# Optimization experiments

Hardware: AMD Instinct MI355X
Metric: run time of the kernel (lower is better)

## Reference

```python
import jax, jax.numpy as jnp
import numpy as np

B, S, HIDDEN = 4, 2048, 1024
NUM_EXPERTS = 8
TOP_K = 4
EPS = 1e-6


def setup_inputs() -> dict:
    key = jax.random.key(0)
    k0, k1, k2 = jax.random.split(key, 3)
    x = jax.random.normal(k0, (B, S, HIDDEN), dtype=jnp.float32)
    Wg = jax.random.normal(k1, (HIDDEN, NUM_EXPERTS), dtype=jnp.float32) * 0.02
    bg = jnp.zeros((NUM_EXPERTS,), dtype=jnp.float32)
    W = jax.random.normal(k2, (NUM_EXPERTS, HIDDEN, HIDDEN), dtype=jnp.float32) * 0.02
    b = jnp.zeros((NUM_EXPERTS, HIDDEN), dtype=jnp.float32)
    return {"x": x, "Wg": Wg, "bg": bg, "W": W, "b": b}


def reference(x, Wg, bg, W, b):
    Bb, Ss, D = x.shape
    xf = x.reshape(-1, D)                       # [T, D]
    T = xf.shape[0]

    # --- router ---
    router_logits = xf @ Wg + bg                # [T, E]
    router_probs = jax.nn.softmax(router_logits, axis=-1)
    top_k_probs, top_k_indices = jax.lax.top_k(router_probs, TOP_K)  # [T, K]
    top_k_weights = top_k_probs / (top_k_probs.sum(axis=-1, keepdims=True) + EPS)
    expert_mask = jax.nn.one_hot(top_k_indices, NUM_EXPERTS, dtype=jnp.float32).sum(axis=1)  # [T, E]

    # --- experts: original computes every expert on every token then masks;
    # same math expressed as one batched GEMM + gather ---
    all_out = jnp.einsum('td,edf->etf', xf, W) + b[:, None, :]  # [E, T, D]
    sel = all_out[top_k_indices.T, jnp.arange(T)[None, :]]      # [K, T, D]
    moe_output = jnp.einsum('tk,ktd->td', top_k_weights, sel).reshape(Bb, Ss, D)

    # --- load-balancing aux loss ---
    aux_loss = jnp.dot(expert_mask.mean(axis=0), router_probs.mean(axis=0)) * NUM_EXPERTS
    return moe_output, aux_loss
```

## Files before the change

### kernel.cpp

```cpp
#include <hip/hip_runtime.h>
#include <hip/hip_bf16.h>

#define T_TOK 8192
#define DH    1024
#define NE    8
#define TK    4

typedef unsigned short u16;
typedef __bf16 bf16x8 __attribute__((ext_vector_type(8)));
typedef float  f32x4  __attribute__((ext_vector_type(4)));

__device__ __forceinline__ u16 f2b(float f) {
    union { float f; unsigned u; } v; v.f = f;
    unsigned u = v.u;
    u += 0x7FFFu + ((u >> 16) & 1u);
    return (u16)(u >> 16);
}
__device__ __forceinline__ float b2f(u16 h) {
    union { unsigned u; float f; } v; v.u = ((unsigned)h) << 16;
    return v.f;
}
__device__ __forceinline__ void glds16(const u16* g, u16* l) {
    __builtin_amdgcn_global_load_lds((const __attribute__((address_space(1))) void*)g,
                                     (__attribute__((address_space(3))) void*)l, 16, 0, 0);
}

#define FENCE() asm volatile("" ::: "memory")
#define SBAR()  do { FENCE(); __builtin_amdgcn_s_barrier(); FENCE(); } while (0)
#define WAITLGKM0() do { asm volatile("s_waitcnt lgkmcnt(0)" ::: "memory"); \
                         __builtin_amdgcn_sched_barrier(0); } while (0)

__global__ __launch_bounds__(256) void cast_w_kernel(const float* __restrict__ W,
                                                     u16* __restrict__ wbt) {
    __shared__ float tile[64][65];
    const int e  = blockIdx.z;
    const int d0 = blockIdx.y * 64;
    const int f0 = blockIdx.x * 64;
    const int r  = threadIdx.x >> 4;
    const int c4 = (threadIdx.x & 15) * 4;
    const float* src = W + ((size_t)e << 20) + (size_t)d0 * DH + f0;
    #pragma unroll
    for (int i = 0; i < 4; i++) {
        const int row = i * 16 + r;
        const float4 v = *(const float4*)(src + (size_t)row * DH + c4);
        tile[row][c4]     = v.x;
        tile[row][c4 + 1] = v.y;
        tile[row][c4 + 2] = v.z;
        tile[row][c4 + 3] = v.w;
    }
    __syncthreads();
    u16* dst = wbt + ((size_t)e << 20) + (size_t)f0 * DH + d0;
    #pragma unroll
    for (int i = 0; i < 4; i++) {
        const int orow = i * 16 + r;
        ushort4 o;
        o.x = f2b(tile[c4][orow]);
        o.y = f2b(tile[c4 + 1][orow]);
        o.z = f2b(tile[c4 + 2][orow]);
        o.w = f2b(tile[c4 + 3][orow]);
        *(ushort4*)(dst + (size_t)orow * DH + c4) = o;
    }
}

__global__ __launch_bounds__(512) void router_kernel(
    const float* __restrict__ x, const float* __restrict__ Wg, const float* __restrict__ bg,
    u16* __restrict__ xb,
    int* __restrict__ bucket_tok, float* __restrict__ bucket_w,
    int* __restrict__ tk_e, float* __restrict__ tk_w,
    int* __restrict__ cnt, float* __restrict__ probsum)
{
    __shared__ int   lcnt[NE];
    __shared__ float lprob[NE];
    __shared__ int   gbase[NE];
    const int tid = threadIdx.x;
    const int wv = tid >> 6, lane = tid & 63;
    const int t = blockIdx.x * 8 + wv;
    if (tid < NE) { lcnt[tid] = 0; lprob[tid] = 0.f; }
    __syncthreads();

    float a[NE] = {};
    {
        const float* xr = x + (size_t)t * DH;
        u16* xbr = xb + (size_t)t * DH;
        #pragma unroll
        for (int it = 0; it < 4; it++) {
            const int d = it * 256 + lane * 4;
            const float4 v = *(const float4*)(xr + d);
            ushort4 o;
            o.x = f2b(v.x); o.y = f2b(v.y); o.z = f2b(v.z); o.w = f2b(v.w);
            *(ushort4*)(xbr + d) = o;
            const float* wr = Wg + d * NE;
            #pragma unroll
            for (int e = 0; e < NE; e++)
                a[e] += v.x * wr[e] + v.y * wr[NE + e] + v.z * wr[2 * NE + e] + v.w * wr[3 * NE + e];
        }
    }
    #pragma unroll
    for (int e = 0; e < NE; e++) {
        float v = a[e];
        #pragma unroll
        for (int off = 32; off > 0; off >>= 1) v += __shfl_down(v, off);
        a[e] = v;
    }

    int idx4[TK]; float w4[TK]; int off4[TK];
    if (lane == 0) {
        float logits[NE], probs[NE];
        float mx = -1e30f;
        #pragma unroll
        for (int e = 0; e < NE; e++) { logits[e] = a[e] + bg[e]; mx = fmaxf(mx, logits[e]); }
        float Z = 0.f;
        #pragma unroll
        for (int e = 0; e < NE; e++) { probs[e] = expf(logits[e] - mx); Z += probs[e]; }
        const float rZ = 1.f / Z;
        #pragma unroll
        for (int e = 0; e < NE; e++) probs[e] *= rZ;

        float rem2[NE];
        #pragma unroll
        for (int e = 0; e < NE; e++) rem2[e] = probs[e];
        float s4 = 0.f;
        #pragma unroll
        for (int k = 0; k < TK; k++) {
            int best = 0; float bv = rem2[0];
            #pragma unroll
            for (int e = 1; e < NE; e++) if (rem2[e] > bv) { bv = rem2[e]; best = e; }
            idx4[k] = best; w4[k] = bv; s4 += bv; rem2[best] = -1e30f;
        }
        const float rs = 1.f / (s4 + 1e-6f);
        #pragma unroll
        for (int k = 0; k < TK; k++) {
            w4[k] *= rs;
            tk_e[t * TK + k] = idx4[k];
            tk_w[t * TK + k] = w4[k];
            off4[k] = atomicAdd(&lcnt[idx4[k]], 1);
        }
        #pragma unroll
        for (int e = 0; e < NE; e++) atomicAdd(&lprob[e], probs[e]);
    }
    __syncthreads();
    if (tid < NE) {
        gbase[tid] = atomicAdd(&cnt[tid], lcnt[tid]);
        atomicAdd(&probsum[tid], lprob[tid]);
    }
    __syncthreads();
    if (lane == 0) {
        #pragma unroll
        for (int k = 0; k < TK; k++) {
            const int e = idx4[k];
            const int slot = gbase[e] + off4[k];
            bucket_tok[e * T_TOK + slot] = (t << 2) | k;
            bucket_w[e * T_TOK + slot]   = w4[k];
        }
    }
}

__global__ __launch_bounds__(512, 2) void moe_gemm_kernel(
    const u16* __restrict__ xb, const u16* __restrict__ wbt,
    const int* __restrict__ bucket_tok, const float* __restrict__ bucket_w,
    const int* __restrict__ cnt, u16* __restrict__ y)
{
    __shared__ u16 As[2][256 * 64];
    __shared__ u16 Bs[2][256 * 64];
    __shared__ int   s_tok[256];
    __shared__ float s_w[256];

    const int tid  = threadIdx.x;
    const int lane = tid & 63;
    const int wid  = tid >> 6;
    const int wr   = wid >> 2;
    const int wc   = wid & 3;
    const int fr   = lane & 15;
    const int fq   = (lane >> 4) * 8;
    const int swz  = (fr & 7) << 3;
    const int gsw  = ((lane & 7) ^ (lane >> 3)) * 8;
    const int crow = lane >> 3;

    for (int vt = blockIdx.x; vt < 1024; vt += 256) {
        const int mb = vt >> 5;
        const int e  = (vt >> 2) & 7;
        const int nb = vt & 3;
        const int M  = cnt[e];
        const int m0 = mb << 8;
        if (m0 >= M) continue;
        const int n0 = nb << 8;

        __syncthreads();
        if (tid < 256) {
            const int slot = m0 + tid;
            if (slot < M) {
                s_tok[tid] = bucket_tok[e * T_TOK + slot];
                s_w[tid]   = bucket_w[e * T_TOK + slot];
            } else { s_tok[tid] = -1; s_w[tid] = 0.f; }
        }
        __syncthreads();

        const u16* gA[4]; const u16* gB[4];
        #pragma unroll
        for (int q = 0; q < 4; q++) {
            const int row = wid * 32 + q * 8 + crow;
            const int tok = s_tok[row];
            gA[q] = xb + (size_t)(tok >= 0 ? (tok >> 2) : 0) * DH + gsw;
            gB[q] = wbt + ((size_t)e << 20) + (size_t)(n0 + row) * DH + gsw;
        }

        f32x4 acc[8][4] = {};

        auto STAGE = [&](int kt) {
            const int p  = kt & 1;
            const int ko = kt * 64;
            #pragma unroll
            for (int q = 0; q < 4; q++)
                glds16(gA[q] + ko, &As[p][(wid * 4 + q) * 512]);
            #pragma unroll
            for (int q = 0; q < 4; q++)
                glds16(gB[q] + ko, &Bs[p][(wid * 4 + q) * 512]);
        };

        STAGE(0); STAGE(1);
        asm volatile("s_waitcnt vmcnt(8)" ::: "memory");
        SBAR();

        const int arow = (wr * 128 + fr) * 64;
        const int brow = (wc * 64  + fr) * 64;
        const int c0 = fq ^ swz;
        const int c1 = (32 + fq) ^ swz;

        bf16x8 afL[4][2], afH[4][2], bfL[2][2], bfH[2][2];

        for (int kt = 0; kt < 16; ++kt) {
            const int p = kt & 1;
            const u16* Ap = &As[p][0];
            const u16* Bp = &Bs[p][0];

            #pragma unroll
            for (int mi = 0; mi < 4; mi++) {
                afL[mi][0] = *(const bf16x8*)&Ap[arow + mi * 1024 + c0];
                afL[mi][1] = *(const bf16x8*)&Ap[arow + mi * 1024 + c1];
            }
            #pragma unroll
            for (int nj = 0; nj < 2; nj++) {
                bfL[nj][0] = *(const bf16x8*)&Bp[brow + nj * 1024 + c0];
                bfL[nj][1] = *(const bf16x8*)&Bp[brow + nj * 1024 + c1];
            }
            SBAR(); WAITLGKM0();
            __builtin_amdgcn_s_setprio(1);
            #pragma unroll
            for (int mi = 0; mi < 4; mi++)
                #pragma unroll
                for (int nj = 0; nj < 2; nj++) {
                    acc[mi][nj] = __builtin_amdgcn_mfma_f32_16x16x32_bf16(afL[mi][0], bfL[nj][0], acc[mi][nj], 0, 0, 0);
                    acc[mi][nj] = __builtin_amdgcn_mfma_f32_16x16x32_bf16(afL[mi][1], bfL[nj][1], acc[mi][nj], 0, 0, 0);
                }
            __builtin_amdgcn_s_setprio(0);
            SBAR();

            #pragma unroll
            for (int nj = 0; nj < 2; nj++) {
                bfH[nj][0] = *(const bf16x8*)&Bp[brow + (nj + 2) * 1024 + c0];
                bfH[nj][1] = *(const bf16x8*)&Bp[brow + (nj + 2) * 1024 + c1];
            }
            SBAR(); WAITLGKM0();
            __builtin_amdgcn_s_setprio(1);
            #pragma unroll
            for (int mi = 0; mi < 4; mi++)
                #pragma unroll
                for (int nj = 0; nj < 2; nj++) {
                    acc[mi][nj + 2] = __builtin_amdgcn_mfma_f32_16x16x32_bf16(afL[mi][0], bfH[nj][0], acc[mi][nj + 2], 0, 0, 0);
                    acc[mi][nj + 2] = __builtin_amdgcn_mfma_f32_16x16x32_bf16(afL[mi][1], bfH[nj][1], acc[mi][nj + 2], 0, 0, 0);
                }
            __builtin_amdgcn_s_setprio(0);
            SBAR();

            #pragma unroll
            for (int mi = 0; mi < 4; mi++) {
                afH[mi][0] = *(const bf16x8*)&Ap[arow + (mi + 4) * 1024 + c0];
                afH[mi][1] = *(const bf16x8*)&Ap[arow + (mi + 4) * 1024 + c1];
            }
            SBAR(); WAITLGKM0();
            __builtin_amdgcn_s_setprio(1);
            #pragma unroll
            for (int mi = 0; mi < 4; mi++)
                #pragma unroll
                for (int nj = 0; nj < 2; nj++) {
                    acc[mi + 4][nj + 2] = __builtin_amdgcn_mfma_f32_16x16x32_bf16(afH[mi][0], bfH[nj][0], acc[mi + 4][nj + 2], 0, 0, 0);
                    acc[mi + 4][nj + 2] = __builtin_amdgcn_mfma_f32_16x16x32_bf16(afH[mi][1], bfH[nj][1], acc[mi + 4][nj + 2], 0, 0, 0);
                }
            __builtin_amdgcn_s_setprio(0);
            SBAR();

            if (kt < 14) STAGE(kt + 2);
            __builtin_amdgcn_s_setprio(1);
            #pragma unroll
            for (int mi = 0; mi < 4; mi++)
                #pragma unroll
                for (int nj = 0; nj < 2; nj++) {
                    acc[mi + 4][nj] = __builtin_amdgcn_mfma_f32_16x16x32_bf16(afH[mi][0], bfL[nj][0], acc[mi + 4][nj], 0, 0, 0);
                    acc[mi + 4][nj] = __builtin_amdgcn_mfma_f32_16x16x32_bf16(afH[mi][1], bfL[nj][1], acc[mi + 4][nj], 0, 0, 0);
                }
            __builtin_amdgcn_s_setprio(0);
            if (kt < 14)       asm volatile("s_waitcnt vmcnt(8)" ::: "memory");
            else if (kt == 14) asm volatile("s_waitcnt vmcnt(0)" ::: "memory");
            SBAR();
        }

        const int cl = lane & 15;
        const int rb = (lane >> 4) * 4;
        #pragma unroll
        for (int mi = 0; mi < 8; mi++) {
            #pragma unroll
            for (int r = 0; r < 4; r++) {
                const int srow = wr * 128 + mi * 16 + rb + r;
                const int tok = s_tok[srow];
                if (tok < 0) continue;
                const float w = s_w[srow];
                u16* yr = y + (size_t)tok * DH + (n0 + wc * 64 + cl);
                #pragma unroll
                for (int nj = 0; nj < 4; nj++)
                    yr[nj * 16] = f2b(acc[mi][nj][r] * w);
            }
        }
    }
}

__global__ __launch_bounds__(256) void combine_kernel(
    const u16* __restrict__ y, const int* __restrict__ tk_e, const float* __restrict__ tk_w,
    const float* __restrict__ bexp,
    const int* __restrict__ cnt, const float* __restrict__ probsum,
    float* __restrict__ out, float* __restrict__ out_aux)
{
    const int t = blockIdx.x;
    const int c = threadIdx.x * 4;
    if (t == 0 && threadIdx.x == 0) {
        float s = 0.f;
        for (int e = 0; e < NE; e++) s += (float)cnt[e] * probsum[e];
        out_aux[0] = s * (float)NE / ((float)T_TOK * (float)T_TOK);
    }
    float o0 = 0.f, o1 = 0.f, o2 = 0.f, o3 = 0.f;
    #pragma unroll
    for (int k = 0; k < TK; k++) {
        const int e   = tk_e[t * TK + k];
        const float w = tk_w[t * TK + k];
        const ushort4 yv = *(const ushort4*)(y + ((size_t)(t * TK + k)) * DH + c);
        const float4  bv = *(const float4*)(bexp + (size_t)e * DH + c);
        o0 += b2f(yv.x) + w * bv.x;
        o1 += b2f(yv.y) + w * bv.y;
        o2 += b2f(yv.z) + w * bv.z;
        o3 += b2f(yv.w) + w * bv.w;
    }
    float4 ov = {o0, o1, o2, o3};
    *(float4*)(out + (size_t)t * DH + c) = ov;
}

extern "C" void kernel_launch(void* const* d_in, const int* in_sizes, int n_in,
                              void* d_out, int out_size, void* d_ws, size_t ws_size,
                              hipStream_t stream)
{
    const float* x  = (const float*)d_in[0];
    const float* Wg = (const float*)d_in[1];
    const float* bg = (const float*)d_in[2];
    const float* W  = (const float*)d_in[3];
    const float* b  = (const float*)d_in[4];
    float* out = (float*)d_out;

    char* ws = (char*)d_ws;
    u16*   xb         = (u16*)(ws);
    u16*   wbt        = (u16*)(ws + 16777216);
    u16*   y          = (u16*)(ws + 33554432);
    int*   bucket_tok = (int*)(ws + 100663296);
    float* bucket_w   = (float*)(ws + 100925440);
    int*   tk_e       = (int*)(ws + 101187584);
    float* tk_w       = (float*)(ws + 101318656);
    int*   cnt        = (int*)(ws + 101449728);
    float* probsum    = (float*)(ws + 101449760);

    hipMemsetAsync(cnt, 0, 64, stream);

    cast_w_kernel<<<dim3(16, 16, NE), 256, 0, stream>>>(W, wbt);
    router_kernel<<<1024, 512, 0, stream>>>(x, Wg, bg, xb, bucket_tok, bucket_w, tk_e, tk_w, cnt, probsum);
    moe_gemm_kernel<<<dim3(256), 512, 0, stream>>>(xb, wbt, bucket_tok, bucket_w, cnt, y);
    combine_kernel<<<8192, 256, 0, stream>>>(y, tk_e, tk_w, b, cnt, probsum, out, out + (size_t)T_TOK * DH);
}
```

Measured before the change: 267.3 us.

## Split tile staging into quadrant loads interleaved across MFMA phases; remap experts per block

The GEMM prefetch is now split into four quadrant-specific global-to-LDS loads (A low/high, B low/high), each issued right after the phase that last reads that quadrant. This spreads memory traffic across the k-loop instead of one burst, with vmcnt waits retuned to match. Blocks are also statically bound to one expert and iterate over four tiles of it, and the router's Wg reads are vectorised to float4. The tighter buffer-reuse timing risks races if a quadrant is overwritten while still being read, and the fixed expert mapping can leave blocks idle when expert counts are uneven.

```diff
diff --git a/kernel.cpp b/kernel.cpp
--- a/kernel.cpp
+++ b/kernel.cpp
@@ -82,6 +82,7 @@
     {
         const float* xr = x + (size_t)t * DH;
         u16* xbr = xb + (size_t)t * DH;
+        const float4* wg = (const float4*)Wg;
         #pragma unroll
         for (int it = 0; it < 4; it++) {
             const int d = it * 256 + lane * 4;
@@ -89,10 +90,18 @@
             ushort4 o;
             o.x = f2b(v.x); o.y = f2b(v.y); o.z = f2b(v.z); o.w = f2b(v.w);
             *(ushort4*)(xbr + d) = o;
-            const float* wr = Wg + d * NE;
-            #pragma unroll
-            for (int e = 0; e < NE; e++)
-                a[e] += v.x * wr[e] + v.y * wr[NE + e] + v.z * wr[2 * NE + e] + v.w * wr[3 * NE + e];
+            const float4 w0l = wg[2 * (d + 0)], w0h = wg[2 * (d + 0) + 1];
+            const float4 w1l = wg[2 * (d + 1)], w1h = wg[2 * (d + 1) + 1];
+            const float4 w2l = wg[2 * (d + 2)], w2h = wg[2 * (d + 2) + 1];
+            const float4 w3l = wg[2 * (d + 3)], w3h = wg[2 * (d + 3) + 1];
+            a[0] += v.x * w0l.x + v.y * w1l.x + v.z * w2l.x + v.w * w3l.x;
+            a[1] += v.x * w0l.y + v.y * w1l.y + v.z * w2l.y + v.w * w3l.y;
+            a[2] += v.x * w0l.z + v.y * w1l.z + v.z * w2l.z + v.w * w3l.z;
+            a[3] += v.x * w0l.w + v.y * w1l.w + v.z * w2l.w + v.w * w3l.w;
+            a[4] += v.x * w0h.x + v.y * w1h.x + v.z * w2h.x + v.w * w3h.x;
+            a[5] += v.x * w0h.y + v.y * w1h.y + v.z * w2h.y + v.w * w3h.y;
+            a[6] += v.x * w0h.z + v.y * w1h.z + v.z * w2h.z + v.w * w3h.z;
+            a[7] += v.x * w0h.w + v.y * w1h.w + v.z * w2h.w + v.w * w3h.w;
         }
     }
     #pragma unroll
@@ -176,11 +185,19 @@
     const int gsw  = ((lane & 7) ^ (lane >> 3)) * 8;
     const int crow = lane >> 3;
 
-    for (int vt = blockIdx.x; vt < 1024; vt += 256) {
-        const int mb = vt >> 5;
-        const int e  = (vt >> 2) & 7;
-        const int nb = vt & 3;
-        const int M  = cnt[e];
+    const int ALb = 2 * wid + (wid >= 4 ? 8 : 0);
+    const int AHb = ALb + 8;
+    const int BLb = (wid >> 1) * 8 + (wid & 1) * 2;
+    const int BHb = BLb + 4;
+
+    const int e = blockIdx.x & 7;
+    const int c = blockIdx.x >> 3;
+    const int M = cnt[e];
+
+    for (int j = 0; j < 4; ++j) {
+        const int idx = j * 32 + c;
+        const int mb = idx >> 2;
+        const int nb = idx & 3;
         const int m0 = mb << 8;
         if (m0 >= M) continue;
         const int n0 = nb << 8;
@@ -195,29 +212,30 @@
         }
         __syncthreads();
 
-        const u16* gA[4]; const u16* gB[4];
-        #pragma unroll
-        for (int q = 0; q < 4; q++) {
-            const int row = wid * 32 + q * 8 + crow;
-            const int tok = s_tok[row];
-            gA[q] = xb + (size_t)(tok >= 0 ? (tok >> 2) : 0) * DH + gsw;
-            gB[q] = wbt + ((size_t)e << 20) + (size_t)(n0 + row) * DH + gsw;
-        }
+        const int rAL0 = ALb * 8 + crow, rAL1 = rAL0 + 8;
+        const int rAH0 = AHb * 8 + crow, rAH1 = rAH0 + 8;
+        const int tAL0 = s_tok[rAL0], tAL1 = s_tok[rAL1];
+        const int tAH0 = s_tok[rAH0], tAH1 = s_tok[rAH1];
+        const u16* gAL0 = xb + (size_t)(tAL0 >= 0 ? (tAL0 >> 2) : 0) * DH + gsw;
+        const u16* gAL1 = xb + (size_t)(tAL1 >= 0 ? (tAL1 >> 2) : 0) * DH + gsw;
+        const u16* gAH0 = xb + (size_t)(tAH0 >= 0 ? (tAH0 >> 2) : 0) * DH + gsw;
+        const u16* gAH1 = xb + (size_t)(tAH1 >= 0 ? (tAH1 >> 2) : 0) * DH + gsw;
+        const u16* wbe  = wbt + ((size_t)e << 20);
+        const u16* gBL0 = wbe + (size_t)(n0 + BLb * 8 + crow) * DH + gsw;
+        const u16* gBL1 = gBL0 + (size_t)8 * DH;
+        const u16* gBH0 = wbe + (size_t)(n0 + BHb * 8 + crow) * DH + gsw;
+        const u16* gBH1 = gBH0 + (size_t)8 * DH;
 
         f32x4 acc[8][4] = {};
 
-        auto STAGE = [&](int kt) {
-            const int p  = kt & 1;
-            const int ko = kt * 64;
-            #pragma unroll
-            for (int q = 0; q < 4; q++)
-                glds16(gA[q] + ko, &As[p][(wid * 4 + q) * 512]);
-            #pragma unroll
-            for (int q = 0; q < 4; q++)
-                glds16(gB[q] + ko, &Bs[p][(wid * 4 + q) * 512]);
-        };
-
-        STAGE(0); STAGE(1);
+        #pragma unroll
+        for (int kt = 0; kt < 2; kt++) {
+            const int ko = kt * 64; const int p = kt;
+            glds16(gAL0 + ko, &As[p][ALb * 512]); glds16(gAL1 + ko, &As[p][(ALb + 1) * 512]);
+            glds16(gAH0 + ko, &As[p][AHb * 512]); glds16(gAH1 + ko, &As[p][(AHb + 1) * 512]);
+            glds16(gBL0 + ko, &Bs[p][BLb * 512]); glds16(gBL1 + ko, &Bs[p][(BLb + 1) * 512]);
+            glds16(gBH0 + ko, &Bs[p][BHb * 512]); glds16(gBH1 + ko, &Bs[p][(BHb + 1) * 512]);
+        }
         asm volatile("s_waitcnt vmcnt(8)" ::: "memory");
         SBAR();
 
@@ -243,6 +261,12 @@
                 bfL[nj][0] = *(const bf16x8*)&Bp[brow + nj * 1024 + c0];
                 bfL[nj][1] = *(const bf16x8*)&Bp[brow + nj * 1024 + c1];
             }
+            if (kt >= 1 && kt <= 14) {
+                const int ko = (kt + 1) * 64; const int q = (kt + 1) & 1;
+                glds16(gAH0 + ko, &As[q][AHb * 512]);
+                glds16(gAH1 + ko, &As[q][(AHb + 1) * 512]);
+            }
+            asm volatile("s_waitcnt lgkmcnt(8)" ::: "memory");
             SBAR(); WAITLGKM0();
             __builtin_amdgcn_s_setprio(1);
             #pragma unroll
@@ -260,6 +284,11 @@
                 bfH[nj][0] = *(const bf16x8*)&Bp[brow + (nj + 2) * 1024 + c0];
                 bfH[nj][1] = *(const bf16x8*)&Bp[brow + (nj + 2) * 1024 + c1];
             }
+            if (kt <= 13) {
+                const int ko = (kt + 2) * 64;
+                glds16(gAL0 + ko, &As[p][ALb * 512]);
+                glds16(gAL1 + ko, &As[p][(ALb + 1) * 512]);
+            }
             SBAR(); WAITLGKM0();
             __builtin_amdgcn_s_setprio(1);
             #pragma unroll
@@ -277,6 +306,11 @@
                 afH[mi][0] = *(const bf16x8*)&Ap[arow + (mi + 4) * 1024 + c0];
                 afH[mi][1] = *(const bf16x8*)&Ap[arow + (mi + 4) * 1024 + c1];
             }
+            if (kt <= 13) {
+                const int ko = (kt + 2) * 64;
+                glds16(gBL0 + ko, &Bs[p][BLb * 512]);
+                glds16(gBL1 + ko, &Bs[p][(BLb + 1) * 512]);
+            }
             SBAR(); WAITLGKM0();
             __builtin_amdgcn_s_setprio(1);
             #pragma unroll
@@ -289,7 +323,11 @@
             __builtin_amdgcn_s_setprio(0);
             SBAR();
 
-            if (kt < 14) STAGE(kt + 2);
+            if (kt <= 13) {
+                const int ko = (kt + 2) * 64;
+                glds16(gBH0 + ko, &Bs[p][BHb * 512]);
+                glds16(gBH1 + ko, &Bs[p][(BHb + 1) * 512]);
+            }
             __builtin_amdgcn_s_setprio(1);
             #pragma unroll
             for (int mi = 0; mi < 4; mi++)
@@ -299,7 +337,7 @@
                     acc[mi + 4][nj] = __builtin_amdgcn_mfma_f32_16x16x32_bf16(afH[mi][1], bfL[nj][1], acc[mi + 4][nj], 0, 0, 0);
                 }
             __builtin_amdgcn_s_setprio(0);
-            if (kt < 14)       asm volatile("s_waitcnt vmcnt(8)" ::: "memory");
+            if (kt <= 13)      asm volatile("s_waitcnt vmcnt(6)" ::: "memory");
             else if (kt == 14) asm volatile("s_waitcnt vmcnt(0)" ::: "memory");
             SBAR();
         }
```

After: 256.4 us. -4.1%, faster.
